# Kernel tuning notes

Hardware: AMD Instinct MI355X
Metric: run time of the kernel (lower is better)

Reference implementation:

```python
import jax, jax.numpy as jnp
import numpy as np
from jax import lax


def setup_inputs() -> dict:
    key = jax.random.key(0)
    ks = jax.random.split(key, 16)
    def rn(k, shape, s=0.05):
        return (jax.random.normal(k, shape) * s).astype(jnp.float32)
    B, N, F = 16, 1024, 200
    return dict(
        x=jax.random.normal(ks[0], (B, 1, N, F), dtype=jnp.float32),
        gat_W=rn(ks[1], (F, F)), att_src=rn(ks[2], (F,)), att_dst=rn(ks[3], (F,)), gat_b=rn(ks[4], (F,)),
        conv1_w=rn(ks[5], (40, 1, 1, 26)), conv1_b=rn(ks[6], (40,)),
        bn1_g=jnp.ones((40,), jnp.float32), bn1_b=jnp.zeros((40,), jnp.float32),
        bn1_m=jnp.zeros((40,), jnp.float32), bn1_v=jnp.ones((40,), jnp.float32),
        conv2_w=rn(ks[7], (40, 40, N), 0.01), conv2_b=rn(ks[8], (40,)),
        bn2_g=jnp.ones((40,), jnp.float32), bn2_b=jnp.zeros((40,), jnp.float32),
        bn2_m=jnp.zeros((40,), jnp.float32), bn2_v=jnp.ones((40,), jnp.float32),
        projc_w=rn(ks[9], (40, 40)), projc_b=rn(ks[10], (40,)),
        W1=rn(ks[11], (1400, 1024)), b1=rn(ks[12], (1024,)),
        W2=rn(ks[13], (1024, 1024)), b2=rn(ks[14], (1024,)),
        ln_g=jnp.ones((1024,), jnp.float32), ln_b=jnp.zeros((1024,), jnp.float32),
    )


def _bn(y, g, b, m, v, eps=1e-5):
    # eval-mode BatchNorm over channel axis 1
    shp = (1, -1) + (1,) * (y.ndim - 2)
    return (y - m.reshape(shp)) * (g.reshape(shp) / jnp.sqrt(v.reshape(shp) + eps)) + b.reshape(shp)


def reference(x, gat_W, att_src, att_dst, gat_b, conv1_w, conv1_b,
              bn1_g, bn1_b, bn1_m, bn1_v, conv2_w, conv2_b,
              bn2_g, bn2_b, bn2_m, bn2_v, projc_w, projc_b,
              W1, b1, W2, b2, ln_g, ln_b):
    B, _, N, F = x.shape  # (16,1,1024,200)
    # --- EEG_GAT (PyG GATConv, heads=1). edge_index only covers nodes 0..N-1;
    # add_self_loops applies to all B*N nodes -> first graph is dense attention
    # (complete graph incl. self), remaining nodes see only their self-loop.
    h = x.reshape(B * N, F) @ gat_W               # (B*N, 200)
    a_s = h[:N] @ att_src                          # source scores, first graph
    a_d = h[:N] @ att_dst                          # target scores
    logits = jax.nn.leaky_relu(a_s[None, :] + a_d[:, None], 0.2)  # [target i, source j]
    out0 = jax.nn.softmax(logits, axis=1) @ h[:N]  # (N, 200)
    gat = (jnp.concatenate([out0, h[N:]], axis=0) + gat_b).reshape(B, 1, N, F)
    x = x + gat  # ResidualAdd (dropout in eval = identity)
    # --- PatchEmbedding shallownet
    y = lax.conv_general_dilated(x, conv1_w, (1, 1), 'VALID',
                                 dimension_numbers=('NCHW', 'OIHW', 'NCHW'))
    y = y + conv1_b[None, :, None, None]           # (B,40,1024,175)
    y = y.reshape(B, 40, N, 35, 5).mean(-1)        # AvgPool2d (1,5) stride (1,5)
    y = jax.nn.elu(_bn(y, bn1_g, bn1_b, bn1_m, bn1_v))
    y = jnp.einsum('bchw,och->bow', y, conv2_w) + conv2_b[None, :, None]  # Conv2d(40,40,(1024,1)) -> (B,40,35)
    y = jax.nn.elu(_bn(y, bn2_g, bn2_b, bn2_m, bn2_v))
    # projection 1x1 conv then rearrange 'b e h w -> b (h w) e' then flatten
    y = jnp.einsum('bow,eo->bew', y, projc_w) + projc_b[None, :, None]
    y = y.transpose(0, 2, 1).reshape(B, -1)        # (B, 1400)
    # --- Proj_eeg
    z = y @ W1 + b1
    z = z + (jax.nn.gelu(z, approximate=False) @ W2 + b2)
    mu = z.mean(-1, keepdims=True)
    var = ((z - mu) ** 2).mean(-1, keepdims=True)
    return (z - mu) / jnp.sqrt(var + 1e-5) * ln_g + ln_b
```

## Files before the change

kernel.cpp:

```cpp
#include <hip/hip_runtime.h>
#include <math.h>

typedef __attribute__((ext_vector_type(8))) short short8;
typedef __attribute__((ext_vector_type(4))) float f32x4;

__device__ __forceinline__ unsigned f2bf(float f) {
  unsigned u = __float_as_uint(f);
  return (u + 0x7FFFu + ((u >> 16) & 1u)) >> 16;
}
__device__ __forceinline__ unsigned pk2(float lo, float hi) {
  return f2bf(lo) | (f2bf(hi) << 16);
}

#define WS_X1    0
#define WS_W2P   3328000
#define WS_AS    4966400
#define WS_AD    4967424
#define WS_WEFB  4968464
#define WS_S1    4969664
#define WS_SH1   4969704
#define WS_S2    4969744
#define WS_SH2   4969784
#define WS_H     4970496
#define WS_P     5232640
#define WS_HT    5494784
#define WS_Y3P   WS_P
#define WS_Y5    8400768
#define WS_ZP    8455936
#define WS_Z2P   8570624
#define WS_WPT   8701696

__global__ __launch_bounds__(256) void k0_prep(const float* __restrict__ gat_W,
                        const float* __restrict__ conv1_w, const float* __restrict__ conv1_b,
                        const float* __restrict__ bn1_g, const float* __restrict__ bn1_b,
                        const float* __restrict__ bn1_m, const float* __restrict__ bn1_v,
                        const float* __restrict__ conv2_b,
                        const float* __restrict__ bn2_g, const float* __restrict__ bn2_b,
                        const float* __restrict__ bn2_m, const float* __restrict__ bn2_v,
                        const float* __restrict__ w2,
                        float* __restrict__ ws) {
  int bx = blockIdx.x, t = threadIdx.x;
  if (bx < 224) {
    unsigned short* wpt = (unsigned short*)(ws + WS_WPT);
    int idx = bx * 256 + t;
    int n = idx / 224, k = idx % 224;
    float v = (n < 200 && k < 200) ? gat_W[k * 200 + n] : 0.f;
    wpt[idx] = (unsigned short)f2bf(v);
    return;
  }
  if (bx == 224) {
    if (t < 48) {
      unsigned short* wb = (unsigned short*)(ws + WS_WEFB);
      float wv[30];
      if (t < 40) {
        for (int j = 0; j < 30; ++j) {
          float s = 0.f;
          for (int tt = 0; tt < 5; ++tt) {
            int k = j - tt;
            if (k >= 0 && k < 26) s += conv1_w[t * 26 + k];
          }
          wv[j] = s * 0.2f;
        }
      }
      for (int k = 0; k < 32; ++k)
        wb[t * 32 + k] = (unsigned short)f2bf((t < 40 && k < 30) ? wv[k] : 0.f);
    }
    if (t < 40) {
      float s1 = bn1_g[t] * rsqrtf(bn1_v[t] + 1e-5f);
      ws[WS_S1 + t] = s1;
      ws[WS_SH1 + t] = bn1_b[t] + (conv1_b[t] - bn1_m[t]) * s1;
      float s2 = bn2_g[t] * rsqrtf(bn2_v[t] + 1e-5f);
      ws[WS_S2 + t] = s2;
      ws[WS_SH2 + t] = bn2_b[t] + (conv2_b[t] - bn2_m[t]) * s2;
    }
    return;
  }
  __shared__ unsigned short lds[2560];
  int q = bx - 225;
  int c8 = q / 6, o0 = (q % 6) * 8;
  unsigned short* w2p = (unsigned short*)(ws + WS_W2P);
#pragma unroll
  for (int i = 0; i < 10; ++i) {
    int e = i * 256 + t;
    int o = e / 320, rr = e % 320;
    int c = rr / 8, nl = rr % 8;
    int oa = o0 + o;
    float v = (oa < 40) ? w2[(oa * 40 + c) * 1024 + c8 * 8 + nl] : 0.f;
    lds[o * 320 + nl * 40 + c] = (unsigned short)f2bf(v);
  }
  __syncthreads();
  uint4* src = (uint4*)lds;
  uint4* dst = (uint4*)(w2p + (c8 * 48 + o0) * 320);
  for (int i = t; i < 320; i += 256) dst[i] = src[i];
}

__global__ __launch_bounds__(256) void k1_mfma(const float* __restrict__ x,
                                               const unsigned short* __restrict__ wpt,
                                               const float* __restrict__ gat_b,
                                               float* __restrict__ h,
                                               unsigned short* __restrict__ hT,
                                               float* __restrict__ x1) {
  __shared__ unsigned short As[64 * 232];
  __shared__ unsigned short Bt[64 * 232];
  int t = threadIdx.x;
  int wave = t >> 6, lane = t & 63;
  int m16 = lane & 15, quad = lane >> 4;
  int row0 = blockIdx.x * 64;
  {
    int m = t >> 2, kq = (t & 3) * 8;
    const float* xr = x + (row0 + m) * 200;
#pragma unroll
    for (int s = 0; s < 7; ++s) {
      int kg = s * 32 + kq;
      uint4 pv;
      if (kg + 8 <= 200) {
        float4 a = *(const float4*)(xr + kg);
        float4 b = *(const float4*)(xr + kg + 4);
        pv.x = pk2(a.x, a.y); pv.y = pk2(a.z, a.w);
        pv.z = pk2(b.x, b.y); pv.w = pk2(b.z, b.w);
      } else {
        float e[8];
#pragma unroll
        for (int q = 0; q < 8; ++q) e[q] = (kg + q < 200) ? xr[kg + q] : 0.f;
        pv.x = pk2(e[0], e[1]); pv.y = pk2(e[2], e[3]);
        pv.z = pk2(e[4], e[5]); pv.w = pk2(e[6], e[7]);
      }
      *(uint4*)&As[m * 232 + kg] = pv;
    }
  }
  __syncthreads();
  for (int c = 0; c < 4; ++c) {
    int n0 = c * 64;
    for (int i = t; i < 1792; i += 256) {
      int row = i / 28, ch = i % 28;
      *(short8*)&Bt[row * 232 + ch * 8] = *(const short8*)&wpt[(n0 + row) * 224 + ch * 8];
    }
    __syncthreads();
    f32x4 acc[4];
#pragma unroll
    for (int nt = 0; nt < 4; ++nt) acc[nt] = (f32x4){0.f, 0.f, 0.f, 0.f};
#pragma unroll
    for (int s = 0; s < 7; ++s) {
      short8 af = *(const short8*)&As[(wave * 16 + m16) * 232 + s * 32 + quad * 8];
      int kb = s * 32 + quad * 8;
#pragma unroll
      for (int nt = 0; nt < 4; ++nt) {
        short8 bf = *(const short8*)&Bt[(nt * 16 + m16) * 232 + kb];
        acc[nt] = __builtin_amdgcn_mfma_f32_16x16x32_bf16(af, bf, acc[nt], 0, 0, 0);
      }
    }
    if (blockIdx.x < 16) {
#pragma unroll
      for (int nt = 0; nt < 4; ++nt) {
        int col = n0 + nt * 16 + m16;
#pragma unroll
        for (int r = 0; r < 4; ++r) {
          int row = row0 + wave * 16 + quad * 4 + r;
          float v = acc[nt][r];
          h[row * 256 + col] = v;
          hT[col * 1024 + row] = (unsigned short)f2bf(v);
        }
      }
    } else {
#pragma unroll
      for (int nt = 0; nt < 4; ++nt) {
        int col = n0 + nt * 16 + m16;
        if (col < 200) {
          float gb = gat_b[col];
#pragma unroll
          for (int r = 0; r < 4; ++r) {
            int row = row0 + wave * 16 + quad * 4 + r;
            x1[row * 200 + col] = x[row * 200 + col] + acc[nt][r] + gb;
          }
        }
      }
    }
    __syncthreads();
  }
}

__global__ __launch_bounds__(256) void k1b_scores(const float* __restrict__ h,
                                                  const float* __restrict__ att_src,
                                                  const float* __restrict__ att_dst,
                                                  float* __restrict__ as_,
                                                  float* __restrict__ ad_) {
  int t = threadIdx.x;
  int wave = t >> 6, lane = t & 63;
  int r = blockIdx.x * 4 + wave;
  float s = 0.f, d = 0.f;
  if (lane < 50) {
    float4 v = *(const float4*)(h + r * 256 + lane * 4);
    float4 a = *(const float4*)(att_src + lane * 4);
    float4 dd = *(const float4*)(att_dst + lane * 4);
    s = v.x * a.x + v.y * a.y + v.z * a.z + v.w * a.w;
    d = v.x * dd.x + v.y * dd.y + v.z * dd.z + v.w * dd.w;
  }
#pragma unroll
  for (int off = 32; off > 0; off >>= 1) {
    s += __shfl_down(s, off);
    d += __shfl_down(d, off);
  }
  if (lane == 0) {
    as_[r] = s;
    ad_[r] = d;
  }
}

__global__ __launch_bounds__(256) void kP(const float* __restrict__ as_,
                                          const float* __restrict__ ad_,
                                          unsigned short* __restrict__ Pb) {
  __shared__ float rb[256];
  int t = threadIdx.x, i = blockIdx.x;
  float a0 = as_[t], a1 = as_[256 + t], a2 = as_[512 + t], a3 = as_[768 + t];
  rb[t] = fmaxf(fmaxf(a0, a1), fmaxf(a2, a3));
  __syncthreads();
  for (int st = 128; st > 0; st >>= 1) {
    if (t < st) rb[t] = fmaxf(rb[t], rb[t + st]);
    __syncthreads();
  }
  float maxs = rb[0];
  __syncthreads();
  float ad = ad_[i];
  float mv = maxs + ad;
  float M = mv >= 0.f ? mv : 0.2f * mv;
  float av[4] = {a0, a1, a2, a3};
  float p[4];
  float s = 0.f;
#pragma unroll
  for (int q = 0; q < 4; ++q) {
    float v = av[q] + ad;
    float l = v >= 0.f ? v : 0.2f * v;
    p[q] = __expf(l - M);
    s += p[q];
  }
  rb[t] = s;
  __syncthreads();
  for (int st = 128; st > 0; st >>= 1) {
    if (t < st) rb[t] += rb[t + st];
    __syncthreads();
  }
  float inv = 1.f / rb[0];
#pragma unroll
  for (int q = 0; q < 4; ++q)
    Pb[i * 1024 + q * 256 + t] = (unsigned short)f2bf(p[q] * inv);
}

__global__ __launch_bounds__(256) void kAttn(const unsigned short* __restrict__ Pb,
                                             const unsigned short* __restrict__ hT,
                                             const float* __restrict__ x,
                                             const float* __restrict__ gat_b,
                                             float* __restrict__ x1) {
  __shared__ float red[4][1024];
  int t = threadIdx.x;
  int wave = t >> 6, lane = t & 63;
  int l15 = lane & 15, quad = lane >> 4;
  int i0 = blockIdx.x * 16, f0 = blockIdx.y * 64;
  int arow = i0 + l15;
  f32x4 acc[4];
#pragma unroll
  for (int nt = 0; nt < 4; ++nt) acc[nt] = (f32x4){0.f, 0.f, 0.f, 0.f};
#pragma unroll
  for (int ks = 0; ks < 8; ++ks) {
    int koff = wave * 256 + ks * 32 + quad * 8;
    short8 a = *(const short8*)&Pb[arow * 1024 + koff];
#pragma unroll
    for (int nt = 0; nt < 4; ++nt) {
      short8 bf = *(const short8*)&hT[(f0 + nt * 16 + l15) * 1024 + koff];
      acc[nt] = __builtin_amdgcn_mfma_f32_16x16x32_bf16(a, bf, acc[nt], 0, 0, 0);
    }
  }
#pragma unroll
  for (int nt = 0; nt < 4; ++nt)
#pragma unroll
    for (int r = 0; r < 4; ++r)
      red[wave][(quad * 4 + r) * 64 + nt * 16 + l15] = acc[nt][r];
  __syncthreads();
#pragma unroll
  for (int e = 0; e < 4; ++e) {
    int idx = t * 4 + e;
    int row = idx >> 6, col = idx & 63;
    int cg = f0 + col;
    if (cg < 200) {
      float s = red[0][idx] + red[1][idx] + red[2][idx] + red[3][idx];
      int rg = i0 + row;
      x1[rg * 200 + cg] = x[rg * 200 + cg] + s + gat_b[cg];
    }
  }
}

__global__ __launch_bounds__(320, 2) void k3_conv(const float* __restrict__ x1,
                                                  const unsigned short* __restrict__ w2pre,
                                                  const unsigned short* __restrict__ weffB,
                                                  const float* __restrict__ ws,
                                                  float* __restrict__ y3p) {
  __shared__ __align__(16) char smem[30016];
  float* xbp = (float*)smem;
  unsigned short* tA = (unsigned short*)(smem + 6400);
  unsigned short* t2 = (unsigned short*)(smem + 6400);
  int t = threadIdx.x;
  int b = blockIdx.x, nc = blockIdx.y;
  int wave = t >> 6, lane = t & 63;
  int l15 = lane & 15, quad = lane >> 4;
  short8 bw[3];
  float s1v[3], sh1v[3];
#pragma unroll
  for (int nt = 0; nt < 3; ++nt) {
    bw[nt] = *(const short8*)&weffB[(nt * 16 + l15) * 32 + quad * 8];
    int c = nt * 16 + l15;
    s1v[nt] = (c < 40) ? ws[WS_S1 + c] : 0.f;
    sh1v[nt] = (c < 40) ? ws[WS_SH1 + c] : 0.f;
  }
  f32x4 acc[3][3];
#pragma unroll
  for (int mt = 0; mt < 3; ++mt)
#pragma unroll
    for (int nt = 0; nt < 3; ++nt) acc[mt][nt] = (f32x4){0.f, 0.f, 0.f, 0.f};
  int mt0 = wave * 4;
  {
    int n0 = nc * 32;
    for (int i = t; i < 400; i += 320) {
      int nn = i / 50, q = i % 50;
      ((float4*)(xbp + nn * 200))[q] = ((const float4*)(x1 + (b * 1024 + n0 + nn) * 200))[q];
    }
  }
  __syncthreads();
  for (int it = 0; it < 4; ++it) {
    int c8 = nc * 4 + it;
    if (t < 280) {
      int nn = t / 35, p = t % 35;
      const float* xr = xbp + nn * 200 + p * 5;
      uint pv[16];
#pragma unroll
      for (int kk = 0; kk < 15; ++kk) pv[kk] = pk2(xr[kk * 2], xr[kk * 2 + 1]);
      pv[15] = 0u;
      uint4* dst = (uint4*)(tA + t * 32);
      dst[0] = make_uint4(pv[0], pv[1], pv[2], pv[3]);
      dst[1] = make_uint4(pv[4], pv[5], pv[6], pv[7]);
      dst[2] = make_uint4(pv[8], pv[9], pv[10], pv[11]);
      dst[3] = make_uint4(pv[12], pv[13], pv[14], pv[15]);
    } else if (t < 288) {
      uint4 z = make_uint4(0u, 0u, 0u, 0u);
      uint4* dst = (uint4*)(tA + t * 32);
      dst[0] = z; dst[1] = z; dst[2] = z; dst[3] = z;
    }
    __syncthreads();
    f32x4 c4[4][3];
#pragma unroll
    for (int mi = 0; mi < 4; ++mi) {
      int row = (mt0 + mi) * 16 + l15;
      row = row > 303 ? 303 : row;
      short8 a = *(const short8*)&tA[row * 32 + quad * 8];
#pragma unroll
      for (int nt = 0; nt < 3; ++nt) {
        f32x4 z = {0.f, 0.f, 0.f, 0.f};
        c4[mi][nt] = __builtin_amdgcn_mfma_f32_16x16x32_bf16(a, bw[nt], z, 0, 0, 0);
      }
    }
    __syncthreads();
#pragma unroll
    for (int mi = 0; mi < 4; ++mi) {
      int mt = mt0 + mi;
#pragma unroll
      for (int nt = 0; nt < 3; ++nt) {
        int c = nt * 16 + l15;
        if (c >= 40) continue;
#pragma unroll
        for (int r = 0; r < 4; ++r) {
          int m = mt * 16 + quad * 4 + r;
          if (m < 280) {
            float v = c4[mi][nt][r] * s1v[nt] + sh1v[nt];
            float e = v > 0.f ? v : __expf(v) - 1.f;
            int p = m % 35, nn = m / 35;
            t2[p * 328 + nn * 40 + c] = (unsigned short)f2bf(e);
          }
        }
      }
    }
    __syncthreads();
    if (it < 3) {
      int n0n = nc * 32 + (it + 1) * 8;
      for (int i = t; i < 400; i += 320) {
        int nn = i / 50, q = i % 50;
        ((float4*)(xbp + nn * 200))[q] = ((const float4*)(x1 + (b * 1024 + n0n + nn) * 200))[q];
      }
    }
    const unsigned short* bbase = w2pre + c8 * 48 * 320;
#pragma unroll
    for (int ks = 0; ks < 2; ++ks) {
      int koff = wave * 64 + ks * 32 + quad * 8;
      short8 a[3], bb[3];
#pragma unroll
      for (int mt = 0; mt < 3; ++mt) {
        int row = mt * 16 + l15;
        row = row > 35 ? 35 : row;
        a[mt] = *(const short8*)&t2[row * 328 + koff];
      }
#pragma unroll
      for (int nt = 0; nt < 3; ++nt)
        bb[nt] = *(const short8*)&bbase[(nt * 16 + l15) * 320 + koff];
#pragma unroll
      for (int mt = 0; mt < 3; ++mt)
#pragma unroll
        for (int nt = 0; nt < 3; ++nt)
          acc[mt][nt] = __builtin_amdgcn_mfma_f32_16x16x32_bf16(a[mt], bb[nt], acc[mt][nt], 0, 0, 0);
    }
    __syncthreads();
  }
  float* red0 = (float*)smem;
  float* red1 = red0 + 48 * 49;
  if (wave < 2) {
    float* r = wave ? red1 : red0;
#pragma unroll
    for (int mt = 0; mt < 3; ++mt)
#pragma unroll
      for (int nt = 0; nt < 3; ++nt)
#pragma unroll
        for (int q = 0; q < 4; ++q)
          r[(mt * 16 + quad * 4 + q) * 49 + nt * 16 + l15] = acc[mt][nt][q];
  }
  __syncthreads();
  if (wave == 2 || wave == 3) {
    float* r = (wave == 3) ? red1 : red0;
#pragma unroll
    for (int mt = 0; mt < 3; ++mt)
#pragma unroll
      for (int nt = 0; nt < 3; ++nt)
#pragma unroll
        for (int q = 0; q < 4; ++q)
          r[(mt * 16 + quad * 4 + q) * 49 + nt * 16 + l15] += acc[mt][nt][q];
  }
  __syncthreads();
  if (wave == 4) {
#pragma unroll
    for (int mt = 0; mt < 3; ++mt)
#pragma unroll
      for (int nt = 0; nt < 3; ++nt)
#pragma unroll
        for (int q = 0; q < 4; ++q)
          red0[(mt * 16 + quad * 4 + q) * 49 + nt * 16 + l15] += acc[mt][nt][q];
  }
  __syncthreads();
  float* dst = y3p + (b * 32 + nc) * 1400;
  for (int idx = t; idx < 1400; idx += 320) {
    int o = idx / 35, p = idx % 35;
    dst[idx] = red0[p * 49 + o] + red1[p * 49 + o];
  }
}

__global__ __launch_bounds__(256) void k4_fused(const float* __restrict__ y3p,
                                                const float* __restrict__ ws,
                                                const float* __restrict__ projc_w,
                                                const float* __restrict__ projc_b,
                                                float* __restrict__ y5) {
  __shared__ float tls[1400];
  int t = threadIdx.x, b = blockIdx.x;
  for (int idx = t; idx < 1400; idx += 256) {
    float s = 0.f;
#pragma unroll 4
    for (int q = 0; q < 32; ++q) s += y3p[(b * 32 + q) * 1400 + idx];
    int o = idx / 35;
    float v = s * ws[WS_S2 + o] + ws[WS_SH2 + o];
    tls[idx] = v > 0.f ? v : __expf(v) - 1.f;
  }
  __syncthreads();
  for (int idx = t; idx < 1400; idx += 256) {
    int p = idx / 40, e = idx % 40;
    float acc = projc_b[e];
    for (int o = 0; o < 40; ++o) acc += tls[o * 35 + p] * projc_w[e * 40 + o];
    y5[b * 1400 + idx] = acc;
  }
}

__global__ __launch_bounds__(256) void k5_fc1(const float* __restrict__ y5,
                                              const float* __restrict__ W1,
                                              float* __restrict__ zp) {
  __shared__ __align__(16) float yls[3200];
  int t = threadIdx.x;
  int nc = blockIdx.x, kc = blockIdx.y;
  for (int i = t; i < 800; i += 256) {
    int bb = i / 50, q = i % 50;
    ((float4*)yls)[bb * 50 + q] = *(const float4*)(y5 + bb * 1400 + kc * 200 + q * 4);
  }
  __syncthreads();
  int nl = t & 31, bg = t >> 5;
  int n = nc * 32 + nl;
  float acc0 = 0.f, acc1 = 0.f;
  const float* y0 = yls + (bg * 2) * 200;
  const float* y1 = yls + (bg * 2 + 1) * 200;
  for (int k = 0; k < 200; ++k) {
    float w = W1[(kc * 200 + k) * 1024 + n];
    acc0 += y0[k] * w;
    acc1 += y1[k] * w;
  }
  zp[(kc * 16 + bg * 2) * 1024 + n] = acc0;
  zp[(kc * 16 + bg * 2 + 1) * 1024 + n] = acc1;
}

__global__ __launch_bounds__(256) void k6_fc2(const float* __restrict__ zp,
                                              const float* __restrict__ b1,
                                              const float* __restrict__ W2,
                                              float* __restrict__ z2p) {
  __shared__ __align__(16) float gls[2048];
  int t = threadIdx.x;
  int nc = blockIdx.x, kc = blockIdx.y;
  for (int i = t; i < 2048; i += 256) {
    int bb = i >> 7, kk = i & 127;
    int np = kc * 128 + kk;
    float s = b1[np];
#pragma unroll
    for (int j = 0; j < 7; ++j) s += zp[(j * 16 + bb) * 1024 + np];
    gls[i] = 0.5f * s * (1.f + erff(s * 0.70710678f));
  }
  __syncthreads();
  int nl = t & 31, bg = t >> 5;
  int n = nc * 32 + nl;
  float acc0 = 0.f, acc1 = 0.f;
  const float* g0 = gls + (bg * 2) * 128;
  const float* g1 = gls + (bg * 2 + 1) * 128;
  for (int k = 0; k < 128; ++k) {
    float w = W2[(kc * 128 + k) * 1024 + n];
    acc0 += g0[k] * w;
    acc1 += g1[k] * w;
  }
  z2p[(kc * 16 + bg * 2) * 1024 + n] = acc0;
  z2p[(kc * 16 + bg * 2 + 1) * 1024 + n] = acc1;
}

__global__ __launch_bounds__(256) void k7_ln(const float* __restrict__ zp,
                                             const float* __restrict__ z2p,
                                             const float* __restrict__ b1,
                                             const float* __restrict__ b2,
                                             const float* __restrict__ ln_g,
                                             const float* __restrict__ ln_b,
                                             float* __restrict__ out) {
  __shared__ float r1[256], r2[256];
  int t = threadIdx.x, b = blockIdx.x;
  float4 v = *(const float4*)(b1 + t * 4);
  float4 bb2 = *(const float4*)(b2 + t * 4);
  v.x += bb2.x; v.y += bb2.y; v.z += bb2.z; v.w += bb2.w;
#pragma unroll
  for (int kc = 0; kc < 7; ++kc) {
    float4 p = *(const float4*)(zp + (kc * 16 + b) * 1024 + t * 4);
    v.x += p.x; v.y += p.y; v.z += p.z; v.w += p.w;
  }
#pragma unroll
  for (int kc = 0; kc < 8; ++kc) {
    float4 p = *(const float4*)(z2p + (kc * 16 + b) * 1024 + t * 4);
    v.x += p.x; v.y += p.y; v.z += p.z; v.w += p.w;
  }
  r1[t] = v.x + v.y + v.z + v.w;
  r2[t] = v.x * v.x + v.y * v.y + v.z * v.z + v.w * v.w;
  __syncthreads();
  for (int s = 128; s > 0; s >>= 1) {
    if (t < s) {
      r1[t] += r1[t + s];
      r2[t] += r2[t + s];
    }
    __syncthreads();
  }
  float mu = r1[0] * (1.f / 1024.f);
  float var = r2[0] * (1.f / 1024.f) - mu * mu;
  float rstd = rsqrtf(var + 1e-5f);
  float4 gg = *(const float4*)(ln_g + t * 4);
  float4 bb = *(const float4*)(ln_b + t * 4);
  float4 o;
  o.x = (v.x - mu) * rstd * gg.x + bb.x;
  o.y = (v.y - mu) * rstd * gg.y + bb.y;
  o.z = (v.z - mu) * rstd * gg.z + bb.z;
  o.w = (v.w - mu) * rstd * gg.w + bb.w;
  *(float4*)(out + b * 1024 + t * 4) = o;
}

extern "C" void kernel_launch(void* const* d_in, const int* in_sizes, int n_in,
                              void* d_out, int out_size, void* d_ws, size_t ws_size,
                              hipStream_t stream) {
  (void)in_sizes; (void)n_in; (void)out_size; (void)ws_size;
  const float* x       = (const float*)d_in[0];
  const float* gat_W   = (const float*)d_in[1];
  const float* att_src = (const float*)d_in[2];
  const float* att_dst = (const float*)d_in[3];
  const float* gat_b   = (const float*)d_in[4];
  const float* conv1_w = (const float*)d_in[5];
  const float* conv2_w = (const float*)d_in[11];
  const float* projc_w = (const float*)d_in[17];
  const float* projc_b = (const float*)d_in[18];
  const float* W1      = (const float*)d_in[19];
  const float* b1      = (const float*)d_in[20];
  const float* W2      = (const float*)d_in[21];
  const float* b2      = (const float*)d_in[22];
  const float* ln_g    = (const float*)d_in[23];
  const float* ln_b    = (const float*)d_in[24];
  float* ws  = (float*)d_ws;
  float* out = (float*)d_out;

  hipLaunchKernelGGL(k0_prep, dim3(993), dim3(256), 0, stream, gat_W, conv1_w,
                     (const float*)d_in[6], (const float*)d_in[7], (const float*)d_in[8],
                     (const float*)d_in[9], (const float*)d_in[10], (const float*)d_in[12],
                     (const float*)d_in[13], (const float*)d_in[14], (const float*)d_in[15],
                     (const float*)d_in[16], conv2_w, ws);
  hipLaunchKernelGGL(k1_mfma, dim3(256), dim3(256), 0, stream, x,
                     (const unsigned short*)(ws + WS_WPT), gat_b, ws + WS_H,
                     (unsigned short*)(ws + WS_HT), ws + WS_X1);
  hipLaunchKernelGGL(k1b_scores, dim3(256), dim3(256), 0, stream, ws + WS_H, att_src, att_dst,
                     ws + WS_AS, ws + WS_AD);
  hipLaunchKernelGGL(kP, dim3(1024), dim3(256), 0, stream, ws + WS_AS, ws + WS_AD,
                     (unsigned short*)(ws + WS_P));
  hipLaunchKernelGGL(kAttn, dim3(64, 4), dim3(256), 0, stream,
                     (const unsigned short*)(ws + WS_P),
                     (const unsigned short*)(ws + WS_HT), x, gat_b, ws + WS_X1);
  hipLaunchKernelGGL(k3_conv, dim3(16, 32), dim3(320), 0, stream, ws + WS_X1,
                     (const unsigned short*)(ws + WS_W2P),
                     (const unsigned short*)(ws + WS_WEFB), ws, ws + WS_Y3P);
  hipLaunchKernelGGL(k4_fused, dim3(16), dim3(256), 0, stream, ws + WS_Y3P, ws, projc_w,
                     projc_b, ws + WS_Y5);
  hipLaunchKernelGGL(k5_fc1, dim3(32, 7), dim3(256), 0, stream, ws + WS_Y5, W1, ws + WS_ZP);
  hipLaunchKernelGGL(k6_fc2, dim3(32, 8), dim3(256), 0, stream, ws + WS_ZP, b1, W2,
                     ws + WS_Z2P);
  hipLaunchKernelGGL(k7_ln, dim3(16), dim3(256), 0, stream, ws + WS_ZP, ws + WS_Z2P, b1, b2,
                     ln_g, ln_b, out);
}
```

Before: 239.9 us.

## Split fused conv kernel into separate conv1 and conv2 kernels via bf16 intermediate

Replaces the fused conv1+pool+BN+ELU+conv2 kernel with two kernels: one computes the pooled conv1 activations per 16-row tile with MFMA and writes them to a bf16 workspace buffer, and the second runs the 1024x40 reduction GEMM with double the K-split (64 chunks) and no shared-memory staging loop or per-iteration barriers. The aim is to remove the many __syncthreads and LDS round trips in the fused loop and raise parallelism. In exchange it adds a global write and reread of an intermediate of about 45 MB in bf16, an extra launch, and twice as many partial sums for the following kernel to reduce.

```diff
diff --git a/kernel.cpp b/kernel.cpp
--- a/kernel.cpp
+++ b/kernel.cpp
@@ -29,6 +29,7 @@
 #define WS_ZP    8455936
 #define WS_Z2P   8570624
 #define WS_WPT   8701696
+#define WS_Y2    8730368
 
 __global__ __launch_bounds__(256) void k0_prep(const float* __restrict__ gat_W,
                         const float* __restrict__ conv1_w, const float* __restrict__ conv1_b,
@@ -288,128 +289,106 @@
   }
 }
 
-__global__ __launch_bounds__(320, 2) void k3_conv(const float* __restrict__ x1,
-                                                  const unsigned short* __restrict__ w2pre,
-                                                  const unsigned short* __restrict__ weffB,
-                                                  const float* __restrict__ ws,
-                                                  float* __restrict__ y3p) {
-  __shared__ __align__(16) char smem[30016];
-  float* xbp = (float*)smem;
-  unsigned short* tA = (unsigned short*)(smem + 6400);
-  unsigned short* t2 = (unsigned short*)(smem + 6400);
-  int t = threadIdx.x;
-  int b = blockIdx.x, nc = blockIdx.y;
+__global__ __launch_bounds__(256) void k3a_conv1(const float* __restrict__ x1,
+                                                 const unsigned short* __restrict__ weffB,
+                                                 const float* __restrict__ ws,
+                                                 unsigned short* __restrict__ y2) {
+  int t = threadIdx.x;
   int wave = t >> 6, lane = t & 63;
   int l15 = lane & 15, quad = lane >> 4;
+  int tile = blockIdx.x * 4 + wave;
+  int row = tile * 16 + l15;
+  int nn = row / 35;
+  int p = row - nn * 35;
   short8 bw[3];
-  float s1v[3], sh1v[3];
+#pragma unroll
+  for (int nt = 0; nt < 3; ++nt)
+    bw[nt] = *(const short8*)&weffB[(nt * 16 + l15) * 32 + quad * 8];
+  const float* xr = x1 + nn * 200 + p * 5;
+  int k0 = quad * 8;
+  float e[8];
+#pragma unroll
+  for (int j = 0; j < 8; ++j) {
+    int k = k0 + j;
+    e[j] = (k < 30) ? xr[k] : 0.f;
+  }
+  short8 xf;
+  ((uint*)&xf)[0] = pk2(e[0], e[1]);
+  ((uint*)&xf)[1] = pk2(e[2], e[3]);
+  ((uint*)&xf)[2] = pk2(e[4], e[5]);
+  ((uint*)&xf)[3] = pk2(e[6], e[7]);
+  unsigned short* yrow = y2 + row * 40;
 #pragma unroll
   for (int nt = 0; nt < 3; ++nt) {
-    bw[nt] = *(const short8*)&weffB[(nt * 16 + l15) * 32 + quad * 8];
-    int c = nt * 16 + l15;
-    s1v[nt] = (c < 40) ? ws[WS_S1 + c] : 0.f;
-    sh1v[nt] = (c < 40) ? ws[WS_SH1 + c] : 0.f;
+    f32x4 z = {0.f, 0.f, 0.f, 0.f};
+    f32x4 c4 = __builtin_amdgcn_mfma_f32_16x16x32_bf16(bw[nt], xf, z, 0, 0, 0);
+    int c0 = nt * 16 + quad * 4;
+    if (c0 < 40) {
+      float4 s1q = *(const float4*)(ws + WS_S1 + c0);
+      float4 sh1q = *(const float4*)(ws + WS_SH1 + c0);
+      float v0 = c4[0] * s1q.x + sh1q.x;
+      float v1 = c4[1] * s1q.y + sh1q.y;
+      float v2 = c4[2] * s1q.z + sh1q.z;
+      float v3 = c4[3] * s1q.w + sh1q.w;
+      v0 = v0 > 0.f ? v0 : __expf(v0) - 1.f;
+      v1 = v1 > 0.f ? v1 : __expf(v1) - 1.f;
+      v2 = v2 > 0.f ? v2 : __expf(v2) - 1.f;
+      v3 = v3 > 0.f ? v3 : __expf(v3) - 1.f;
+      uint2 pv;
+      pv.x = pk2(v0, v1);
+      pv.y = pk2(v2, v3);
+      *(uint2*)&yrow[c0] = pv;
+    }
+  }
+}
+
+__global__ __launch_bounds__(256) void k3b_conv2(const unsigned short* __restrict__ y2,
+                                                 const unsigned short* __restrict__ w2pre,
+                                                 float* __restrict__ y3p) {
+  __shared__ float red[2][48 * 49];
+  int t = threadIdx.x;
+  int wave = t >> 6, lane = t & 63;
+  int l15 = lane & 15, quad = lane >> 4;
+  int b = blockIdx.x, kc = blockIdx.y;
+  const unsigned short* Ab = y2 + (b * 1024 + kc * 16) * 1400;
+  int pA[3];
+#pragma unroll
+  for (int mt = 0; mt < 3; ++mt) {
+    int p = mt * 16 + l15;
+    pA[mt] = p > 34 ? 34 : p;
   }
   f32x4 acc[3][3];
 #pragma unroll
   for (int mt = 0; mt < 3; ++mt)
 #pragma unroll
     for (int nt = 0; nt < 3; ++nt) acc[mt][nt] = (f32x4){0.f, 0.f, 0.f, 0.f};
-  int mt0 = wave * 4;
-  {
-    int n0 = nc * 32;
-    for (int i = t; i < 400; i += 320) {
-      int nn = i / 50, q = i % 50;
-      ((float4*)(xbp + nn * 200))[q] = ((const float4*)(x1 + (b * 1024 + n0 + nn) * 200))[q];
-    }
-  }
-  __syncthreads();
-  for (int it = 0; it < 4; ++it) {
-    int c8 = nc * 4 + it;
-    if (t < 280) {
-      int nn = t / 35, p = t % 35;
-      const float* xr = xbp + nn * 200 + p * 5;
-      uint pv[16];
-#pragma unroll
-      for (int kk = 0; kk < 15; ++kk) pv[kk] = pk2(xr[kk * 2], xr[kk * 2 + 1]);
-      pv[15] = 0u;
-      uint4* dst = (uint4*)(tA + t * 32);
-      dst[0] = make_uint4(pv[0], pv[1], pv[2], pv[3]);
-      dst[1] = make_uint4(pv[4], pv[5], pv[6], pv[7]);
-      dst[2] = make_uint4(pv[8], pv[9], pv[10], pv[11]);
-      dst[3] = make_uint4(pv[12], pv[13], pv[14], pv[15]);
-    } else if (t < 288) {
-      uint4 z = make_uint4(0u, 0u, 0u, 0u);
-      uint4* dst = (uint4*)(tA + t * 32);
-      dst[0] = z; dst[1] = z; dst[2] = z; dst[3] = z;
-    }
-    __syncthreads();
-    f32x4 c4[4][3];
-#pragma unroll
-    for (int mi = 0; mi < 4; ++mi) {
-      int row = (mt0 + mi) * 16 + l15;
-      row = row > 303 ? 303 : row;
-      short8 a = *(const short8*)&tA[row * 32 + quad * 8];
-#pragma unroll
-      for (int nt = 0; nt < 3; ++nt) {
-        f32x4 z = {0.f, 0.f, 0.f, 0.f};
-        c4[mi][nt] = __builtin_amdgcn_mfma_f32_16x16x32_bf16(a, bw[nt], z, 0, 0, 0);
-      }
-    }
-    __syncthreads();
-#pragma unroll
-    for (int mi = 0; mi < 4; ++mi) {
-      int mt = mt0 + mi;
-#pragma unroll
-      for (int nt = 0; nt < 3; ++nt) {
-        int c = nt * 16 + l15;
-        if (c >= 40) continue;
-#pragma unroll
-        for (int r = 0; r < 4; ++r) {
-          int m = mt * 16 + quad * 4 + r;
-          if (m < 280) {
-            float v = c4[mi][nt][r] * s1v[nt] + sh1v[nt];
-            float e = v > 0.f ? v : __expf(v) - 1.f;
-            int p = m % 35, nn = m / 35;
-            t2[p * 328 + nn * 40 + c] = (unsigned short)f2bf(e);
-          }
-        }
-      }
-    }
-    __syncthreads();
-    if (it < 3) {
-      int n0n = nc * 32 + (it + 1) * 8;
-      for (int i = t; i < 400; i += 320) {
-        int nn = i / 50, q = i % 50;
-        ((float4*)(xbp + nn * 200))[q] = ((const float4*)(x1 + (b * 1024 + n0n + nn) * 200))[q];
-      }
-    }
-    const unsigned short* bbase = w2pre + c8 * 48 * 320;
-#pragma unroll
-    for (int ks = 0; ks < 2; ++ks) {
-      int koff = wave * 64 + ks * 32 + quad * 8;
-      short8 a[3], bb[3];
-#pragma unroll
-      for (int mt = 0; mt < 3; ++mt) {
-        int row = mt * 16 + l15;
-        row = row > 35 ? 35 : row;
-        a[mt] = *(const short8*)&t2[row * 328 + koff];
-      }
+#pragma unroll
+  for (int j = 0; j < 5; ++j) {
+    int klocal = wave * 160 + j * 32 + quad * 8;
+    int noff = klocal / 40;
+    int c = klocal - noff * 40;
+    const unsigned short* Ak = Ab + noff * 1400 + c;
+    short8 a[3];
+#pragma unroll
+    for (int mt = 0; mt < 3; ++mt)
+      a[mt] = *(const short8*)&Ak[pA[mt] * 40];
+    int kg = kc * 640 + klocal;
+    int slab = kg >> 8;
+    slab = kg / 320;
+    int kl = kg - slab * 320;
+    const unsigned short* Bb = w2pre + slab * 48 * 320 + kl;
+    short8 bb[3];
+#pragma unroll
+    for (int nt = 0; nt < 3; ++nt)
+      bb[nt] = *(const short8*)&Bb[(nt * 16 + l15) * 320];
+#pragma unroll
+    for (int mt = 0; mt < 3; ++mt)
 #pragma unroll
       for (int nt = 0; nt < 3; ++nt)
-        bb[nt] = *(const short8*)&bbase[(nt * 16 + l15) * 320 + koff];
-#pragma unroll
-      for (int mt = 0; mt < 3; ++mt)
-#pragma unroll
-        for (int nt = 0; nt < 3; ++nt)
-          acc[mt][nt] = __builtin_amdgcn_mfma_f32_16x16x32_bf16(a[mt], bb[nt], acc[mt][nt], 0, 0, 0);
-    }
-    __syncthreads();
-  }
-  float* red0 = (float*)smem;
-  float* red1 = red0 + 48 * 49;
+        acc[mt][nt] = __builtin_amdgcn_mfma_f32_16x16x32_bf16(a[mt], bb[nt], acc[mt][nt], 0, 0, 0);
+  }
   if (wave < 2) {
-    float* r = wave ? red1 : red0;
+    float* r = red[wave];
 #pragma unroll
     for (int mt = 0; mt < 3; ++mt)
 #pragma unroll
@@ -419,8 +398,8 @@
           r[(mt * 16 + quad * 4 + q) * 49 + nt * 16 + l15] = acc[mt][nt][q];
   }
   __syncthreads();
-  if (wave == 2 || wave == 3) {
-    float* r = (wave == 3) ? red1 : red0;
+  if (wave >= 2) {
+    float* r = red[wave - 2];
 #pragma unroll
     for (int mt = 0; mt < 3; ++mt)
 #pragma unroll
@@ -430,20 +409,10 @@
           r[(mt * 16 + quad * 4 + q) * 49 + nt * 16 + l15] += acc[mt][nt][q];
   }
   __syncthreads();
-  if (wave == 4) {
-#pragma unroll
-    for (int mt = 0; mt < 3; ++mt)
-#pragma unroll
-      for (int nt = 0; nt < 3; ++nt)
-#pragma unroll
-        for (int q = 0; q < 4; ++q)
-          red0[(mt * 16 + quad * 4 + q) * 49 + nt * 16 + l15] += acc[mt][nt][q];
-  }
-  __syncthreads();
-  float* dst = y3p + (b * 32 + nc) * 1400;
-  for (int idx = t; idx < 1400; idx += 320) {
+  float* dst = y3p + (b * 64 + kc) * 1400;
+  for (int idx = t; idx < 1400; idx += 256) {
     int o = idx / 35, p = idx % 35;
-    dst[idx] = red0[p * 49 + o] + red1[p * 49 + o];
+    dst[idx] = red[0][p * 49 + o] + red[1][p * 49 + o];
   }
 }
 
@@ -457,7 +426,7 @@
   for (int idx = t; idx < 1400; idx += 256) {
     float s = 0.f;
 #pragma unroll 4
-    for (int q = 0; q < 32; ++q) s += y3p[(b * 32 + q) * 1400 + idx];
+    for (int q = 0; q < 64; ++q) s += y3p[(b * 64 + q) * 1400 + idx];
     int o = idx / 35;
     float v = s * ws[WS_S2 + o] + ws[WS_SH2 + o];
     tls[idx] = v > 0.f ? v : __expf(v) - 1.f;
@@ -608,9 +577,12 @@
   hipLaunchKernelGGL(kAttn, dim3(64, 4), dim3(256), 0, stream,
                      (const unsigned short*)(ws + WS_P),
                      (const unsigned short*)(ws + WS_HT), x, gat_b, ws + WS_X1);
-  hipLaunchKernelGGL(k3_conv, dim3(16, 32), dim3(320), 0, stream, ws + WS_X1,
-                     (const unsigned short*)(ws + WS_W2P),
-                     (const unsigned short*)(ws + WS_WEFB), ws, ws + WS_Y3P);
+  hipLaunchKernelGGL(k3a_conv1, dim3(8960), dim3(256), 0, stream, ws + WS_X1,
+                     (const unsigned short*)(ws + WS_WEFB), ws,
+                     (unsigned short*)(ws + WS_Y2));
+  hipLaunchKernelGGL(k3b_conv2, dim3(16, 64), dim3(256), 0, stream,
+                     (const unsigned short*)(ws + WS_Y2),
+                     (const unsigned short*)(ws + WS_W2P), ws + WS_Y3P);
   hipLaunchKernelGGL(k4_fused, dim3(16), dim3(256), 0, stream, ws + WS_Y3P, ws, projc_w,
                      projc_b, ws + WS_Y5);
   hipLaunchKernelGGL(k5_fc1, dim3(32, 7), dim3(256), 0, stream, ws + WS_Y5, W1, ws + WS_ZP);
```

New measurement: 252.1 us. 1.05x slower.
